# Kernel tuning notes

Measured on AMD Instinct MI355X. Metric: run time of the kernel, lower is better.

The kernel has to match this reference:

```python
import jax, jax.numpy as jnp
import numpy as np

H = 16  # hidden_dim
EPS = 1e-5


def _lstm_layer(x, W_ih, W_hh, b_ih, b_hh):
    # x: [B,T,D_in] -> [B,T,H]; PyTorch gate order i,f,g,o
    B = x.shape[0]
    xg = jnp.einsum('btd,gd->btg', x, W_ih) + (b_ih + b_hh)  # [B,T,4H]

    def step(carry, xt):
        h, c = carry
        gates = xt + h @ W_hh.T
        i, f, g, o = jnp.split(gates, 4, axis=-1)
        c = jax.nn.sigmoid(f) * c + jax.nn.sigmoid(i) * jnp.tanh(g)
        h = jax.nn.sigmoid(o) * jnp.tanh(c)
        return (h, c), h

    h0 = jnp.zeros((B, H), x.dtype)
    _, hs = jax.lax.scan(step, (h0, h0), jnp.swapaxes(xg, 0, 1))  # [T,B,H]
    return jnp.swapaxes(hs, 0, 1)


def setup_inputs() -> dict:
    key = jax.random.key(0)
    ks = jax.random.split(key, 20)
    B, T, D, O = 256, 2048, 57, 4
    x = jax.random.normal(ks[0], (B, T, D), dtype=jnp.float32)
    lengths = jnp.maximum(jnp.sort(jax.random.randint(ks[1], (B,), 1, T + 1))[::-1], 1)
    s = 1.0 / np.sqrt(H)
    u = lambda k, shp: jax.random.uniform(k, shp, jnp.float32, -s, s)
    inp = {'x': x, 'lengths': lengths}
    dims_in = [D, H, H]
    for l in range(3):
        inp[f'W_ih{l}'] = u(ks[2 + 4 * l], (4 * H, dims_in[l]))
        inp[f'W_hh{l}'] = u(ks[3 + 4 * l], (4 * H, H))
        inp[f'b_ih{l}'] = u(ks[4 + 4 * l], (4 * H,))
        inp[f'b_hh{l}'] = u(ks[5 + 4 * l], (4 * H,))
    inp['bn_gamma'] = jnp.ones((H,), jnp.float32)
    inp['bn_beta'] = jnp.zeros((H,), jnp.float32)
    inp['fc_w'] = u(ks[14], (O, H))
    inp['fc_b'] = u(ks[15], (O,))
    return inp


def reference(x, lengths, W_ih0, W_hh0, b_ih0, b_hh0, W_ih1, W_hh1, b_ih1, b_hh1,
              W_ih2, W_hh2, b_ih2, b_hh2, bn_gamma, bn_beta, fc_w, fc_b):
    B, T, _ = x.shape
    h = x
    for W_ih, W_hh, b_ih, b_hh in ((W_ih0, W_hh0, b_ih0, b_hh0),
                                    (W_ih1, W_hh1, b_ih1, b_hh1),
                                    (W_ih2, W_hh2, b_ih2, b_hh2)):
        h = _lstm_layer(h, W_ih, W_hh, b_ih, b_hh)
    # pad_packed_sequence: zero out positions past each sequence length
    mask = (jnp.arange(T)[None, :] < lengths[:, None])[:, :, None].astype(h.dtype)
    h = h * mask  # [B,T,H]
    # BatchNorm1d (training mode) over (batch,time) per channel, incl. padding zeros
    mean = jnp.mean(h, axis=(0, 1))
    var = jnp.mean((h - mean) ** 2, axis=(0, 1))
    norm = (h - mean) * jax.lax.rsqrt(var + EPS) * bn_gamma + bn_beta
    return norm @ fc_w.T + fc_b  # [B,T,4]
```

## Files before the change

### kernel.cpp

```cpp
#include <hip/hip_runtime.h>
#include <math.h>

#define TT 2048
#define BBATCH 256
#define DDIM 57
#define NROWS (BBATCH*TT)
#define NF 524288.0f
#define U 8

#define K1 (-1.4426950408889634f)
#define K2 (-2.8853900817779268f)

__device__ __forceinline__ float bcastl(float v, int k) {
  return __uint_as_float((unsigned)__builtin_amdgcn_readlane((int)__float_as_uint(v), k));
}
__device__ __forceinline__ float rcpf(float x) { return __builtin_amdgcn_rcpf(x); }
__device__ __forceinline__ float exp2f_(float x) { return __builtin_amdgcn_exp2f(x); }

template<int PAT>
__device__ __forceinline__ float quadb(float v) {
  return __int_as_float(__builtin_amdgcn_update_dpp(0, __float_as_int(v), PAT, 0xF, 0xF, true));
}

__global__ void zero_accum_k(float* accum) {
  accum[threadIdx.x] = 0.f;
}

__global__ __launch_bounds__(256) void xg0_gemm_k(
    const float* __restrict__ x, const float* __restrict__ Wih,
    const float* __restrict__ bih, const float* __restrict__ bhh,
    float* __restrict__ xg0)
{
  const int lane = threadIdx.x & 63;
  const int g = (lane & 3) * 16 + (lane >> 2);
  const float fac = ((lane & 3) == 2) ? K2 : K1;
  const int wid  = blockIdx.x * (blockDim.x >> 6) + (threadIdx.x >> 6);
  const int nw   = gridDim.x * (blockDim.x >> 6);
  float w[DDIM];
  #pragma unroll
  for (int d = 0; d < DDIM; ++d) w[d] = fac * Wih[g*DDIM + d];
  const float bias = fac * (bih[g] + bhh[g]);

  int r = wid;
  float xv = 0.f;
  if (r < NROWS && lane < DDIM)
    xv = x[(size_t)__builtin_amdgcn_readfirstlane(r) * DDIM + lane];
  for (; r < NROWS; r += nw) {
    const int rn = r + nw;
    float xn = 0.f;
    if (rn < NROWS && lane < DDIM)
      xn = x[(size_t)__builtin_amdgcn_readfirstlane(rn) * DDIM + lane];
    float a0 = bias, a1 = 0.f, a2 = 0.f, a3 = 0.f;
    #pragma unroll
    for (int d = 0; d < 56; d += 4) {
      a0 += w[d]   * bcastl(xv, d);
      a1 += w[d+1] * bcastl(xv, d+1);
      a2 += w[d+2] * bcastl(xv, d+2);
      a3 += w[d+3] * bcastl(xv, d+3);
    }
    a0 += w[56] * bcastl(xv, 56);
    xg0[(size_t)__builtin_amdgcn_readfirstlane(r) * 64 + lane] = (a0 + a1) + (a2 + a3);
    xv = xn;
  }
}

__global__ __launch_bounds__(192, 1) void lstm_scan_pipe_k(
    const float* __restrict__ xg0,
    const int*   __restrict__ lengths,
    const float* __restrict__ Whh0,
    const float* __restrict__ Wih1, const float* __restrict__ Whh1,
    const float* __restrict__ bih1, const float* __restrict__ bhh1,
    const float* __restrict__ Wih2, const float* __restrict__ Whh2,
    const float* __restrict__ bih2, const float* __restrict__ bhh2,
    float* __restrict__ h2buf, float* __restrict__ accum)
{
  const int tid  = threadIdx.x;
  const int wave = tid >> 6;
  const int lane = tid & 63;
  const int gt   = lane & 3;
  const int ch   = lane >> 2;
  const int g    = gt*16 + ch;
  const int b    = blockIdx.x;
  const int len  = lengths[b];
  const bool isg = (gt == 2);
  const float fac = isg ? K2 : K1;
  const float mg = isg ? 2.f : 1.f;
  const float ag = isg ? -1.f : 0.f;

  __shared__ float lds_h0[2][U][16];
  __shared__ float lds_h1[2][U][16];

  float wa[16], wb[16];
  float bias = 0.f;
  if (wave == 0) {
    #pragma unroll
    for (int k = 0; k < 16; ++k) { wb[k] = fac * Whh0[g*16 + k]; wa[k] = 0.f; }
  } else if (wave == 1) {
    #pragma unroll
    for (int k = 0; k < 16; ++k) { wa[k] = fac * Wih1[g*16 + k]; wb[k] = fac * Whh1[g*16 + k]; }
    bias = fac * (bih1[g] + bhh1[g]);
  } else {
    #pragma unroll
    for (int k = 0; k < 16; ++k) { wa[k] = fac * Wih2[g*16 + k]; wb[k] = fac * Whh2[g*16 + k]; }
    bias = fac * (bih2[g] + bhh2[g]);
  }

  float hs = 0.f, csK = 0.f;
  float sum = 0.f, sq = 0.f;
  const int base = b*TT*64 + lane;
  float* __restrict__ h2row = h2buf + (size_t)b*TT*16;

  auto lstm_update = [&](float dot) {
    float s   = rcpf(1.f + exp2f_(dot));
    float act = fmaf(s, mg, ag);
    float gi = quadb<0x00>(act);
    float gf = quadb<0x55>(act);
    float gg = quadb<0xAA>(act);
    float go = quadb<0xFF>(act);
    csK = fmaf(gf, csK, (K2 * gg) * gi);
    float r = rcpf(1.f + exp2f_(csK));
    hs = go * fmaf(2.f, r, -1.f);
  };
  auto owndot = [&](float seed) {
    float hb[16];
    #pragma unroll
    for (int k = 0; k < 16; ++k) hb[k] = bcastl(hs, 4*k);
    float a0 = seed, a1 = 0.f, a2 = 0.f, a3 = 0.f;
    #pragma unroll
    for (int k = 0; k < 16; k += 4) {
      a0 += wb[k]   * hb[k];
      a1 += wb[k+1] * hb[k+1];
      a2 += wb[k+2] * hb[k+2];
      a3 += wb[k+3] * hb[k+3];
    }
    return (a0 + a1) + (a2 + a3);
  };
  auto indot = [&](const float* hin) {
    float a0 = bias, a1 = 0.f, a2 = 0.f, a3 = 0.f;
    #pragma unroll
    for (int k = 0; k < 16; k += 4) {
      a0 += wa[k]   * hin[k];
      a1 += wa[k+1] * hin[k+1];
      a2 += wa[k+2] * hin[k+2];
      a3 += wa[k+3] * hin[k+3];
    }
    return (a0 + a1) + (a2 + a3);
  };

  const int NS = (len + U - 1) / U;
  const int S  = NS + 2;

  float cur[U], nxt[U];
  if (wave == 0) {
    #pragma unroll
    for (int j = 0; j < U; ++j) cur[j] = xg0[base + j*64];
    #pragma unroll
    for (int j = 0; j < U; ++j) {
      int ip = U + j; ip = ip > TT-1 ? TT-1 : ip;
      nxt[j] = xg0[base + ip*64];
    }
  }

  for (int s = 0; s < S; ++s) {
    const int p = s & 1, q = p ^ 1;
    if (wave == 0) {
      if (s < NS) {
        float ld[U];
        #pragma unroll
        for (int j = 0; j < U; ++j) {
          int ip = (s + 2)*U + j; ip = ip > TT-1 ? TT-1 : ip;
          ld[j] = xg0[base + ip*64];
        }
        #pragma unroll
        for (int j = 0; j < U; ++j) {
          lstm_update(owndot(cur[j]));
          if (gt == 0) lds_h0[p][j][ch] = hs;
        }
        #pragma unroll
        for (int j = 0; j < U; ++j) { cur[j] = nxt[j]; nxt[j] = ld[j]; }
      }
    } else if (wave == 1) {
      if (s >= 1 && s <= NS) {
        float xin[U];
        #pragma unroll
        for (int j = 0; j < U; ++j) {
          const float4* hp = (const float4*)&lds_h0[q][j][0];
          float4 h0v = hp[0], h1v = hp[1], h2v = hp[2], h3v = hp[3];
          float hin[16] = {h0v.x,h0v.y,h0v.z,h0v.w, h1v.x,h1v.y,h1v.z,h1v.w,
                           h2v.x,h2v.y,h2v.z,h2v.w, h3v.x,h3v.y,h3v.z,h3v.w};
          xin[j] = indot(hin);
        }
        #pragma unroll
        for (int j = 0; j < U; ++j) {
          lstm_update(owndot(xin[j]));
          if (gt == 0) lds_h1[p][j][ch] = hs;
        }
      }
    } else {
      if (s >= 2) {
        float xin[U];
        #pragma unroll
        for (int j = 0; j < U; ++j) {
          const float4* hp = (const float4*)&lds_h1[q][j][0];
          float4 h0v = hp[0], h1v = hp[1], h2v = hp[2], h3v = hp[3];
          float hin[16] = {h0v.x,h0v.y,h0v.z,h0v.w, h1v.x,h1v.y,h1v.z,h1v.w,
                           h2v.x,h2v.y,h2v.z,h2v.w, h3v.x,h3v.y,h3v.z,h3v.w};
          xin[j] = indot(hin);
        }
        #pragma unroll
        for (int j = 0; j < U; ++j) {
          lstm_update(owndot(xin[j]));
          const int t = (s - 2)*U + j;
          if (t < len) {
            if (gt == 0) h2row[t*16 + ch] = hs;
            sum += hs; sq += hs*hs;
          }
        }
      }
    }
    __syncthreads();
  }

  for (int idx = len*16 + tid; idx < TT*16; idx += 192)
    h2row[idx] = 0.f;

  if (wave == 2 && gt == 0) {
    atomicAdd(&accum[ch],      sum);
    atomicAdd(&accum[16 + ch], sq);
  }
}

__global__ void prep_k(const float* __restrict__ accum,
                       const float* __restrict__ gamma, const float* __restrict__ beta,
                       const float* __restrict__ fcw, const float* __restrict__ fcb,
                       float* __restrict__ coef)
{
  const int lane = threadIdx.x;
  const int o = lane >> 4, c = lane & 15;
  const float inv_n = 1.0f / NF;
  float mean = accum[c] * inv_n;
  float var  = accum[16 + c] * inv_n - mean*mean;
  float s  = gamma[c] * rsqrtf(var + 1e-5f);
  float tb = beta[c] - mean * s;
  float woc = fcw[o*16 + c];
  coef[lane] = s * woc;
  float term = tb * woc;
  #pragma unroll
  for (int off = 1; off < 16; off <<= 1) term += __shfl_xor(term, off, 16);
  if (c == 0) coef[64 + o] = fcb[o] + term;
}

__global__ __launch_bounds__(256) void finalize_k(
    const float* __restrict__ h2buf, const float* __restrict__ coef,
    float* __restrict__ out)
{
  const int r = blockIdx.x * 256 + threadIdx.x;
  const float4* hp = (const float4*)(h2buf + (size_t)r * 16);
  float4 v0 = hp[0], v1 = hp[1], v2 = hp[2], v3 = hp[3];
  float hv[16] = {v0.x,v0.y,v0.z,v0.w, v1.x,v1.y,v1.z,v1.w,
                  v2.x,v2.y,v2.z,v2.w, v3.x,v3.y,v3.z,v3.w};
  float4 o4;
  float* op = &o4.x;
  #pragma unroll
  for (int o = 0; o < 4; ++o) {
    float a = coef[64 + o];
    #pragma unroll
    for (int c = 0; c < 16; ++c) a += coef[o*16 + c] * hv[c];
    op[o] = a;
  }
  ((float4*)out)[r] = o4;
}

extern "C" void kernel_launch(void* const* d_in, const int* in_sizes, int n_in,
                              void* d_out, int out_size, void* d_ws, size_t ws_size,
                              hipStream_t stream)
{
  const float* x     = (const float*)d_in[0];
  const int* lengths = (const int*)d_in[1];
  const float* W_ih0 = (const float*)d_in[2];
  const float* W_hh0 = (const float*)d_in[3];
  const float* b_ih0 = (const float*)d_in[4];
  const float* b_hh0 = (const float*)d_in[5];
  const float* W_ih1 = (const float*)d_in[6];
  const float* W_hh1 = (const float*)d_in[7];
  const float* b_ih1 = (const float*)d_in[8];
  const float* b_hh1 = (const float*)d_in[9];
  const float* W_ih2 = (const float*)d_in[10];
  const float* W_hh2 = (const float*)d_in[11];
  const float* b_ih2 = (const float*)d_in[12];
  const float* b_hh2 = (const float*)d_in[13];
  const float* gamma = (const float*)d_in[14];
  const float* beta  = (const float*)d_in[15];
  const float* fcw   = (const float*)d_in[16];
  const float* fcb   = (const float*)d_in[17];
  float* out = (float*)d_out;

  float* ws    = (float*)d_ws;
  float* xg0   = ws;
  float* h2    = ws + 33554432;
  float* accum = ws + 33554432 + 8388608;
  float* coef  = accum + 32;

  hipLaunchKernelGGL(zero_accum_k, dim3(1), dim3(32), 0, stream, accum);
  hipLaunchKernelGGL(xg0_gemm_k, dim3(2048), dim3(256), 0, stream,
                     x, W_ih0, b_ih0, b_hh0, xg0);
  hipLaunchKernelGGL(lstm_scan_pipe_k, dim3(256), dim3(192), 0, stream,
                     xg0, lengths, W_hh0, W_ih1, W_hh1, b_ih1, b_hh1,
                     W_ih2, W_hh2, b_ih2, b_hh2, h2, accum);
  hipLaunchKernelGGL(prep_k, dim3(1), dim3(64), 0, stream,
                     accum, gamma, beta, fcw, fcb, coef);
  hipLaunchKernelGGL(finalize_k, dim3(2048), dim3(256), 0, stream, h2, coef, out);
}
```

Before: 694.1 us.

## Fuse layer-0 input projection into the LSTM scan with two producer waves

Removes the separate xg0 GEMM kernel and its 128MB intermediate buffer. Two extra waves per block compute the layer-0 input projection from x on the fly and stage it in LDS, double-buffered one stage ahead of the recurrence wave. The unroll depth grows from 8 to 16 steps per stage, which halves the number of block barriers, and the tanh scaling constants are folded into the gate activation. In exchange the block grows to 320 threads and the projection now shares the critical-path SM with the sequential scan; pipeline latency and register pressure from U=16 may also increase.

```diff
diff --git a/kernel.cpp b/kernel.cpp
--- a/kernel.cpp
+++ b/kernel.cpp
@@ -6,7 +6,7 @@
 #define DDIM 57
 #define NROWS (BBATCH*TT)
 #define NF 524288.0f
-#define U 8
+#define U 16
 
 #define K1 (-1.4426950408889634f)
 #define K2 (-2.8853900817779268f)
@@ -26,48 +26,11 @@
   accum[threadIdx.x] = 0.f;
 }
 
-__global__ __launch_bounds__(256) void xg0_gemm_k(
-    const float* __restrict__ x, const float* __restrict__ Wih,
-    const float* __restrict__ bih, const float* __restrict__ bhh,
-    float* __restrict__ xg0)
-{
-  const int lane = threadIdx.x & 63;
-  const int g = (lane & 3) * 16 + (lane >> 2);
-  const float fac = ((lane & 3) == 2) ? K2 : K1;
-  const int wid  = blockIdx.x * (blockDim.x >> 6) + (threadIdx.x >> 6);
-  const int nw   = gridDim.x * (blockDim.x >> 6);
-  float w[DDIM];
-  #pragma unroll
-  for (int d = 0; d < DDIM; ++d) w[d] = fac * Wih[g*DDIM + d];
-  const float bias = fac * (bih[g] + bhh[g]);
-
-  int r = wid;
-  float xv = 0.f;
-  if (r < NROWS && lane < DDIM)
-    xv = x[(size_t)__builtin_amdgcn_readfirstlane(r) * DDIM + lane];
-  for (; r < NROWS; r += nw) {
-    const int rn = r + nw;
-    float xn = 0.f;
-    if (rn < NROWS && lane < DDIM)
-      xn = x[(size_t)__builtin_amdgcn_readfirstlane(rn) * DDIM + lane];
-    float a0 = bias, a1 = 0.f, a2 = 0.f, a3 = 0.f;
-    #pragma unroll
-    for (int d = 0; d < 56; d += 4) {
-      a0 += w[d]   * bcastl(xv, d);
-      a1 += w[d+1] * bcastl(xv, d+1);
-      a2 += w[d+2] * bcastl(xv, d+2);
-      a3 += w[d+3] * bcastl(xv, d+3);
-    }
-    a0 += w[56] * bcastl(xv, 56);
-    xg0[(size_t)__builtin_amdgcn_readfirstlane(r) * 64 + lane] = (a0 + a1) + (a2 + a3);
-    xv = xn;
-  }
-}
-
-__global__ __launch_bounds__(192, 1) void lstm_scan_pipe_k(
-    const float* __restrict__ xg0,
+__global__ __launch_bounds__(320, 1) void lstm_scan_pipe_k(
+    const float* __restrict__ x,
     const int*   __restrict__ lengths,
-    const float* __restrict__ Whh0,
+    const float* __restrict__ Wih0, const float* __restrict__ Whh0,
+    const float* __restrict__ bih0, const float* __restrict__ bhh0,
     const float* __restrict__ Wih1, const float* __restrict__ Whh1,
     const float* __restrict__ bih1, const float* __restrict__ bhh1,
     const float* __restrict__ Wih2, const float* __restrict__ Whh2,
@@ -84,14 +47,17 @@
   const int len  = lengths[b];
   const bool isg = (gt == 2);
   const float fac = isg ? K2 : K1;
-  const float mg = isg ? 2.f : 1.f;
-  const float ag = isg ? -1.f : 0.f;
+  const float mg = isg ? (2.f*K2) : 1.f;
+  const float ag = isg ? (-K2)    : 0.f;
 
   __shared__ float lds_h0[2][U][16];
   __shared__ float lds_h1[2][U][16];
+  __shared__ float lds_xg[2][U][64];
 
   float wa[16], wb[16];
   float bias = 0.f;
+  float hw[DDIM];
+  float hbias = 0.f;
   if (wave == 0) {
     #pragma unroll
     for (int k = 0; k < 16; ++k) { wb[k] = fac * Whh0[g*16 + k]; wa[k] = 0.f; }
@@ -99,15 +65,18 @@
     #pragma unroll
     for (int k = 0; k < 16; ++k) { wa[k] = fac * Wih1[g*16 + k]; wb[k] = fac * Whh1[g*16 + k]; }
     bias = fac * (bih1[g] + bhh1[g]);
-  } else {
+  } else if (wave == 2) {
     #pragma unroll
     for (int k = 0; k < 16; ++k) { wa[k] = fac * Wih2[g*16 + k]; wb[k] = fac * Whh2[g*16 + k]; }
     bias = fac * (bih2[g] + bhh2[g]);
+  } else {
+    #pragma unroll
+    for (int d = 0; d < DDIM; ++d) hw[d] = fac * Wih0[g*DDIM + d];
+    hbias = fac * (bih0[g] + bhh0[g]);
   }
 
   float hs = 0.f, csK = 0.f;
   float sum = 0.f, sq = 0.f;
-  const int base = b*TT*64 + lane;
   float* __restrict__ h2row = h2buf + (size_t)b*TT*16;
 
   auto lstm_update = [&](float dot) {
@@ -117,9 +86,10 @@
     float gf = quadb<0x55>(act);
     float gg = quadb<0xAA>(act);
     float go = quadb<0xFF>(act);
-    csK = fmaf(gf, csK, (K2 * gg) * gi);
+    float go2 = go + go;
+    csK = fmaf(gf, csK, gg * gi);
     float r = rcpf(1.f + exp2f_(csK));
-    hs = go * fmaf(2.f, r, -1.f);
+    hs = fmaf(go2, r, -go);
   };
   auto owndot = [&](float seed) {
     float hb[16];
@@ -146,38 +116,53 @@
     }
     return (a0 + a1) + (a2 + a3);
   };
+  auto xdot = [&](float xv) {
+    float a0 = hbias, a1 = 0.f, a2 = 0.f, a3 = 0.f;
+    #pragma unroll
+    for (int d = 0; d < 56; d += 4) {
+      a0 += hw[d]   * bcastl(xv, d);
+      a1 += hw[d+1] * bcastl(xv, d+1);
+      a2 += hw[d+2] * bcastl(xv, d+2);
+      a3 += hw[d+3] * bcastl(xv, d+3);
+    }
+    a0 += hw[56] * bcastl(xv, 56);
+    return (a0 + a1) + (a2 + a3);
+  };
 
   const int NS = (len + U - 1) / U;
   const int S  = NS + 2;
 
-  float cur[U], nxt[U];
-  if (wave == 0) {
-    #pragma unroll
-    for (int j = 0; j < U; ++j) cur[j] = xg0[base + j*64];
-    #pragma unroll
-    for (int j = 0; j < U; ++j) {
-      int ip = U + j; ip = ip > TT-1 ? TT-1 : ip;
-      nxt[j] = xg0[base + ip*64];
-    }
-  }
+  float xcur[8];
+  const int hj = (wave - 3) * 8;
+  if (wave >= 3) {
+    #pragma unroll
+    for (int k = 0; k < 8; ++k) {
+      const int t = hj + k;
+      xcur[k] = (lane < DDIM) ? x[(size_t)(b*TT + t)*DDIM + lane] : 0.f;
+    }
+    #pragma unroll
+    for (int k = 0; k < 8; ++k)
+      lds_xg[1][hj + k][lane] = xdot(xcur[k]);
+    #pragma unroll
+    for (int k = 0; k < 8; ++k) {
+      int t = U + hj + k; t = t > TT-1 ? TT-1 : t;
+      xcur[k] = (lane < DDIM) ? x[(size_t)(b*TT + t)*DDIM + lane] : 0.f;
+    }
+  }
+  __syncthreads();
 
   for (int s = 0; s < S; ++s) {
     const int p = s & 1, q = p ^ 1;
     if (wave == 0) {
       if (s < NS) {
-        float ld[U];
-        #pragma unroll
-        for (int j = 0; j < U; ++j) {
-          int ip = (s + 2)*U + j; ip = ip > TT-1 ? TT-1 : ip;
-          ld[j] = xg0[base + ip*64];
-        }
+        float cur[U];
+        #pragma unroll
+        for (int j = 0; j < U; ++j) cur[j] = lds_xg[q][j][lane];
         #pragma unroll
         for (int j = 0; j < U; ++j) {
           lstm_update(owndot(cur[j]));
           if (gt == 0) lds_h0[p][j][ch] = hs;
         }
-        #pragma unroll
-        for (int j = 0; j < U; ++j) { cur[j] = nxt[j]; nxt[j] = ld[j]; }
       }
     } else if (wave == 1) {
       if (s >= 1 && s <= NS) {
@@ -196,7 +181,7 @@
           if (gt == 0) lds_h1[p][j][ch] = hs;
         }
       }
-    } else {
+    } else if (wave == 2) {
       if (s >= 2) {
         float xin[U];
         #pragma unroll
@@ -217,11 +202,30 @@
           }
         }
       }
+    } else {
+      float ld[8];
+      const bool doload = (s + 2 < NS);
+      if (doload) {
+        #pragma unroll
+        for (int k = 0; k < 8; ++k) {
+          int t = (s + 2)*U + hj + k; t = t > TT-1 ? TT-1 : t;
+          ld[k] = (lane < DDIM) ? x[(size_t)(b*TT + t)*DDIM + lane] : 0.f;
+        }
+      }
+      if (s + 1 < NS) {
+        #pragma unroll
+        for (int k = 0; k < 8; ++k)
+          lds_xg[p][hj + k][lane] = xdot(xcur[k]);
+      }
+      if (doload) {
+        #pragma unroll
+        for (int k = 0; k < 8; ++k) xcur[k] = ld[k];
+      }
     }
     __syncthreads();
   }
 
-  for (int idx = len*16 + tid; idx < TT*16; idx += 192)
+  for (int idx = len*16 + tid; idx < TT*16; idx += 320)
     h2row[idx] = 0.f;
 
   if (wave == 2 && gt == 0) {
@@ -296,16 +300,14 @@
   float* out = (float*)d_out;
 
   float* ws    = (float*)d_ws;
-  float* xg0   = ws;
-  float* h2    = ws + 33554432;
-  float* accum = ws + 33554432 + 8388608;
+  float* h2    = ws;
+  float* accum = ws + 8388608;
   float* coef  = accum + 32;
 
   hipLaunchKernelGGL(zero_accum_k, dim3(1), dim3(32), 0, stream, accum);
-  hipLaunchKernelGGL(xg0_gemm_k, dim3(2048), dim3(256), 0, stream,
-                     x, W_ih0, b_ih0, b_hh0, xg0);
-  hipLaunchKernelGGL(lstm_scan_pipe_k, dim3(256), dim3(192), 0, stream,
-                     xg0, lengths, W_hh0, W_ih1, W_hh1, b_ih1, b_hh1,
+  hipLaunchKernelGGL(lstm_scan_pipe_k, dim3(256), dim3(320), 0, stream,
+                     x, lengths, W_ih0, W_hh0, b_ih0, b_hh0,
+                     W_ih1, W_hh1, b_ih1, b_hh1,
                      W_ih2, W_hh2, b_ih2, b_hh2, h2, accum);
   hipLaunchKernelGGL(prep_k, dim3(1), dim3(64), 0, stream,
                      accum, gamma, beta, fcw, fcb, coef);
```

New measurement: 1.156 ms. 66.6% more time.
